# Kernel optimization log

Hardware: AMD Instinct MI355X
Metric: run time of the kernel (lower is better)

Reference implementation:

```python
import jax, jax.numpy as jnp
import numpy as np

D = 768    # text_feature_dim (BERT)
H = 1024   # hidden_dim
L = 16384  # history length


def setup_inputs() -> dict:
    key = jax.random.key(0)
    ks = jax.random.split(key, 10)
    text_v = jax.random.normal(ks[0], (1, D), dtype=jnp.float32)
    result = jax.random.uniform(ks[1], (1,), dtype=jnp.float32)
    text_s = jax.random.normal(ks[2], (L, D), dtype=jnp.float32)
    hidden_s = jax.random.normal(ks[3], (L, H), dtype=jnp.float32)
    # GRU params (PyTorch layout: W_ih [3H, 2D], W_hh [3H, H]), uniform(-1/sqrt(H), 1/sqrt(H))
    s = 1.0 / np.sqrt(H)
    W_ih = jax.random.uniform(ks[4], (3 * H, 2 * D), minval=-s, maxval=s, dtype=jnp.float32)
    W_hh = jax.random.uniform(ks[5], (3 * H, H), minval=-s, maxval=s, dtype=jnp.float32)
    b_ih = jax.random.uniform(ks[6], (3 * H,), minval=-s, maxval=s, dtype=jnp.float32)
    b_hh = jax.random.uniform(ks[7], (3 * H,), minval=-s, maxval=s, dtype=jnp.float32)
    # score layer: Linear(D+H, 1)
    s2 = 1.0 / np.sqrt(D + H)
    score_W = jax.random.uniform(ks[8], (1, D + H), minval=-s2, maxval=s2, dtype=jnp.float32)
    score_b = jax.random.uniform(ks[9], (1,), minval=-s2, maxval=s2, dtype=jnp.float32)
    return {"text_v": text_v, "result": result, "text_s": text_s, "hidden_s": hidden_s,
            "W_ih": W_ih, "W_hh": W_hh, "b_ih": b_ih, "b_hh": b_hh,
            "score_W": score_W, "score_b": score_b}


def reference(text_v, result, text_s, hidden_s, W_ih, W_hh, b_ih, b_hh, score_W, score_b):
    # --- attention over growing history ---
    h = hidden_s[-1:, :]                                   # [1, H] last hidden state
    alpha = jax.nn.softmax(text_s @ text_v.T, axis=0)      # [L, 1]
    attn_h = alpha.T @ hidden_s                            # [1, H]

    # --- score prediction ---
    pred_v = jnp.concatenate([text_v, attn_h], axis=1)     # [1, D+H]
    score = pred_v @ score_W.T + score_b                   # [1, 1]

    # --- input gating by correctness ---
    zeros = jnp.zeros_like(text_v)
    x_r = jnp.where(result >= 0.5,
                    jnp.concatenate([text_v, zeros], axis=1),
                    jnp.concatenate([zeros, text_v], axis=1))  # [1, 2D]

    # --- GRU cell (PyTorch gate order: r, z, n) ---
    gi = x_r @ W_ih.T + b_ih                               # [1, 3H]
    gh = h @ W_hh.T + b_hh                                 # [1, 3H]
    i_r, i_z, i_n = jnp.split(gi, 3, axis=1)
    h_r, h_z, h_n = jnp.split(gh, 3, axis=1)
    r = jax.nn.sigmoid(i_r + h_r)
    z = jax.nn.sigmoid(i_z + h_z)
    n = jnp.tanh(i_n + r * h_n)
    h_new = (1.0 - z) * n + z * h                          # [1, H]

    return score[0], h_new                                 # score.squeeze(0) -> [1]
```

## Files before the change

kernel.cpp:

```cpp
#include <hip/hip_runtime.h>
#include <math.h>

#define LL 16384
#define Dm 768
#define Hm 1024

#define WS_DOTS  0
#define WS_STATS 16384
#define WS_GI    16400
#define WS_GH    19472
#define WS_PART  24576
#define WS_PART2 (24576 + 512*1024)

__device__ __forceinline__ float dot4(float4 a, float4 b) {
    return a.x*b.x + a.y*b.y + a.z*b.z + a.w*b.w;
}

__global__ __launch_bounds__(256) void k_dots_gigh(
    const float* __restrict__ text_v, const float* __restrict__ result,
    const float* __restrict__ text_s, const float* __restrict__ hidden_s,
    const float* __restrict__ W_ih, const float* __restrict__ W_hh,
    const float* __restrict__ b_ih, const float* __restrict__ b_hh,
    float* __restrict__ ws)
{
    const int tid  = threadIdx.x;
    const int lane = tid & 63;
    const int wv   = tid >> 6;
    const int b    = blockIdx.x;

    if (b < 1024) {
        const int wave_g = b*4 + wv;
        float4 tv0 = *(const float4*)(text_v + 4*lane);
        float4 tv1 = *(const float4*)(text_v + 4*lane + 256);
        float4 tv2 = *(const float4*)(text_v + 4*lane + 512);
        #pragma unroll
        for (int r = 0; r < 4; ++r) {
            const int row = wave_g*4 + r;
            const float* p = text_s + (size_t)row*Dm + 4*lane;
            float4 x0 = *(const float4*)(p);
            float4 x1 = *(const float4*)(p + 256);
            float4 x2 = *(const float4*)(p + 512);
            float s = dot4(x0, tv0) + dot4(x1, tv1) + dot4(x2, tv2);
            #pragma unroll
            for (int o = 32; o; o >>= 1) s += __shfl_xor(s, o);
            if (lane == 0) ws[WS_DOTS + row] = s;
        }
    } else if (b < 1216) {
        const int wave_g = (b - 1024)*4 + wv;
        const int off = (result[0] >= 0.5f) ? 0 : Dm;
        float4 tv0 = *(const float4*)(text_v + 4*lane);
        float4 tv1 = *(const float4*)(text_v + 4*lane + 256);
        float4 tv2 = *(const float4*)(text_v + 4*lane + 512);
        #pragma unroll
        for (int r = 0; r < 4; ++r) {
            const int k = wave_g*4 + r;
            const float* p = W_ih + (size_t)k*(2*Dm) + off + 4*lane;
            float4 x0 = *(const float4*)(p);
            float4 x1 = *(const float4*)(p + 256);
            float4 x2 = *(const float4*)(p + 512);
            float s = dot4(x0, tv0) + dot4(x1, tv1) + dot4(x2, tv2);
            #pragma unroll
            for (int o = 32; o; o >>= 1) s += __shfl_xor(s, o);
            if (lane == 0) ws[WS_GI + k] = s + b_ih[k];
        }
    } else {
        const int wave_g = (b - 1216)*4 + wv;
        const float* h = hidden_s + (size_t)(LL - 1)*Hm;
        float4 h0 = *(const float4*)(h + 4*lane);
        float4 h1 = *(const float4*)(h + 4*lane + 256);
        float4 h2 = *(const float4*)(h + 4*lane + 512);
        float4 h3 = *(const float4*)(h + 4*lane + 768);
        #pragma unroll
        for (int r = 0; r < 4; ++r) {
            const int k = wave_g*4 + r;
            const float* p = W_hh + (size_t)k*Hm + 4*lane;
            float4 x0 = *(const float4*)(p);
            float4 x1 = *(const float4*)(p + 256);
            float4 x2 = *(const float4*)(p + 512);
            float4 x3 = *(const float4*)(p + 768);
            float s = dot4(x0, h0) + dot4(x1, h1) + dot4(x2, h2) + dot4(x3, h3);
            #pragma unroll
            for (int o = 32; o; o >>= 1) s += __shfl_xor(s, o);
            if (lane == 0) ws[WS_GH + k] = s + b_hh[k];
        }
    }
}

__global__ __launch_bounds__(1024) void k_stats(float* __restrict__ ws) {
    __shared__ float red[16];
    __shared__ float s_m;
    const int tid = threadIdx.x;
    const float* dots = ws + WS_DOTS;
    float v[16];
    float m = -1e30f;
    #pragma unroll
    for (int k = 0; k < 16; ++k) { v[k] = dots[tid + k*1024]; m = fmaxf(m, v[k]); }
    #pragma unroll
    for (int o = 32; o; o >>= 1) m = fmaxf(m, __shfl_xor(m, o));
    if ((tid & 63) == 0) red[tid >> 6] = m;
    __syncthreads();
    if (tid == 0) {
        float mm = red[0];
        #pragma unroll
        for (int i = 1; i < 16; ++i) mm = fmaxf(mm, red[i]);
        s_m = mm;
    }
    __syncthreads();
    m = s_m;
    float s = 0.f;
    #pragma unroll
    for (int k = 0; k < 16; ++k) s += expf(v[k] - m);
    #pragma unroll
    for (int o = 32; o; o >>= 1) s += __shfl_xor(s, o);
    if ((tid & 63) == 0) red[tid >> 6] = s;
    __syncthreads();
    if (tid == 0) {
        float ss = 0.f;
        #pragma unroll
        for (int i = 0; i < 16; ++i) ss += red[i];
        ws[WS_STATS]     = s_m;
        ws[WS_STATS + 1] = 1.0f / ss;
    }
}

__global__ __launch_bounds__(256) void k_wsum(
    const float* __restrict__ hidden_s, float* __restrict__ ws)
{
    const int p = blockIdx.x;
    const int t = threadIdx.x;
    const float m   = ws[WS_STATS];
    const float inv = ws[WS_STATS + 1];
    float4 acc = {0.f, 0.f, 0.f, 0.f};
    const int row0 = p*32;
    for (int r = 0; r < 32; ++r) {
        const int row = row0 + r;
        const float w = expf(ws[WS_DOTS + row] - m) * inv;
        const float4 hv = *(const float4*)(hidden_s + (size_t)row*Hm + 4*t);
        acc.x += w*hv.x; acc.y += w*hv.y; acc.z += w*hv.z; acc.w += w*hv.w;
    }
    *(float4*)(ws + WS_PART + p*1024 + 4*t) = acc;
}

__global__ __launch_bounds__(256) void k_reduce(float* __restrict__ ws) {
    const int b = blockIdx.x;
    const int t = threadIdx.x;
    float4 acc = {0.f, 0.f, 0.f, 0.f};
    for (int r = 0; r < 32; ++r) {
        const float4 v = *(const float4*)(ws + WS_PART + (size_t)(b*32 + r)*1024 + 4*t);
        acc.x += v.x; acc.y += v.y; acc.z += v.z; acc.w += v.w;
    }
    *(float4*)(ws + WS_PART2 + b*1024 + 4*t) = acc;
}

__global__ __launch_bounds__(1024) void k_final(
    const float* __restrict__ text_v, const float* __restrict__ hidden_s,
    const float* __restrict__ score_W, const float* __restrict__ score_b,
    float* __restrict__ ws, float* __restrict__ out)
{
    __shared__ float sred[16];
    const int tid = threadIdx.x;
    float a = 0.f;
    #pragma unroll
    for (int r = 0; r < 16; ++r) a += ws[WS_PART2 + r*1024 + tid];
    float sp = a * score_W[Dm + tid];
    if (tid < Dm) sp += text_v[tid] * score_W[tid];
    #pragma unroll
    for (int o = 32; o; o >>= 1) sp += __shfl_xor(sp, o);
    if ((tid & 63) == 0) sred[tid >> 6] = sp;
    __syncthreads();
    if (tid == 0) {
        float s = score_b[0];
        #pragma unroll
        for (int i = 0; i < 16; ++i) s += sred[i];
        out[0] = s;
    }
    const float gi_r = ws[WS_GI + tid];
    const float gi_z = ws[WS_GI + 1024 + tid];
    const float gi_n = ws[WS_GI + 2048 + tid];
    const float gh_r = ws[WS_GH + tid];
    const float gh_z = ws[WS_GH + 1024 + tid];
    const float gh_n = ws[WS_GH + 2048 + tid];
    const float hprev = hidden_s[(size_t)(LL - 1)*Hm + tid];
    const float r = 1.f / (1.f + expf(-(gi_r + gh_r)));
    const float z = 1.f / (1.f + expf(-(gi_z + gh_z)));
    const float n = tanhf(gi_n + r*gh_n);
    out[1 + tid] = (1.f - z)*n + z*hprev;
}

extern "C" void kernel_launch(void* const* d_in, const int* in_sizes, int n_in,
                              void* d_out, int out_size, void* d_ws, size_t ws_size,
                              hipStream_t stream) {
    const float* text_v   = (const float*)d_in[0];
    const float* result   = (const float*)d_in[1];
    const float* text_s   = (const float*)d_in[2];
    const float* hidden_s = (const float*)d_in[3];
    const float* W_ih     = (const float*)d_in[4];
    const float* W_hh     = (const float*)d_in[5];
    const float* b_ih     = (const float*)d_in[6];
    const float* b_hh     = (const float*)d_in[7];
    const float* score_W  = (const float*)d_in[8];
    const float* score_b  = (const float*)d_in[9];
    float* out = (float*)d_out;
    float* ws  = (float*)d_ws;

    k_dots_gigh<<<1408, 256, 0, stream>>>(text_v, result, text_s, hidden_s,
                                          W_ih, W_hh, b_ih, b_hh, ws);
    k_stats <<<1,   1024, 0, stream>>>(ws);
    k_wsum  <<<512, 256,  0, stream>>>(hidden_s, ws);
    k_reduce<<<16,  256,  0, stream>>>(ws);
    k_final <<<1,   1024, 0, stream>>>(text_v, hidden_s, score_W, score_b, ws, out);
}
```

Before: 192.2 us.

## Fuse attention dots and weighted sum with online-softmax partial reductions

Replaces the global two-pass softmax (dots kernel, stats kernel, weighted-sum kernel) with a flash-style online softmax. Each block computes dots for its 32 rows, a local max and exp-weights, and the weighted hidden-state sum in one pass, storing partial max, sum and vector. The partials are then merged hierarchically with rescaling in the mid and final kernels. This removes two launches and the global round trip of the dot products, and lets text_s and hidden_s reads share one kernel. The GI/GH block counts are also rebalanced to fewer blocks with more rows each.

```diff
diff --git a/kernel.cpp b/kernel.cpp
--- a/kernel.cpp
+++ b/kernel.cpp
@@ -5,55 +5,84 @@
 #define Dm 768
 #define Hm 1024
 
-#define WS_DOTS  0
-#define WS_STATS 16384
-#define WS_GI    16400
-#define WS_GH    19472
-#define WS_PART  24576
-#define WS_PART2 (24576 + 512*1024)
+#define ATT_B 512
+#define GI_B  48
+#define GH_B  64
+
+#define WS_GI 0
+#define WS_GH 3072
+#define WS_PM 6144
+#define WS_PS 6656
+#define WS_PV 7168
+#define WS_M2 (7168 + 512*1024)
+#define WS_S2 (WS_M2 + 16)
+#define WS_V2 (WS_S2 + 16)
 
 __device__ __forceinline__ float dot4(float4 a, float4 b) {
     return a.x*b.x + a.y*b.y + a.z*b.z + a.w*b.w;
 }
 
-__global__ __launch_bounds__(256) void k_dots_gigh(
+__global__ __launch_bounds__(256) void k_main(
     const float* __restrict__ text_v, const float* __restrict__ result,
     const float* __restrict__ text_s, const float* __restrict__ hidden_s,
     const float* __restrict__ W_ih, const float* __restrict__ W_hh,
     const float* __restrict__ b_ih, const float* __restrict__ b_hh,
     float* __restrict__ ws)
 {
+    const int b    = blockIdx.x;
     const int tid  = threadIdx.x;
     const int lane = tid & 63;
     const int wv   = tid >> 6;
-    const int b    = blockIdx.x;
-
-    if (b < 1024) {
-        const int wave_g = b*4 + wv;
+
+    if (b < ATT_B) {
+        __shared__ float dots[32];
+        __shared__ float wts[32];
+        const int row0 = b * 32;
         float4 tv0 = *(const float4*)(text_v + 4*lane);
         float4 tv1 = *(const float4*)(text_v + 4*lane + 256);
         float4 tv2 = *(const float4*)(text_v + 4*lane + 512);
         #pragma unroll
-        for (int r = 0; r < 4; ++r) {
-            const int row = wave_g*4 + r;
-            const float* p = text_s + (size_t)row*Dm + 4*lane;
+        for (int i = 0; i < 8; ++i) {
+            const int rl = wv*8 + i;
+            const float* p = text_s + (size_t)(row0 + rl)*Dm + 4*lane;
             float4 x0 = *(const float4*)(p);
             float4 x1 = *(const float4*)(p + 256);
             float4 x2 = *(const float4*)(p + 512);
             float s = dot4(x0, tv0) + dot4(x1, tv1) + dot4(x2, tv2);
             #pragma unroll
             for (int o = 32; o; o >>= 1) s += __shfl_xor(s, o);
-            if (lane == 0) ws[WS_DOTS + row] = s;
-        }
-    } else if (b < 1216) {
-        const int wave_g = (b - 1024)*4 + wv;
+            if (lane == 0) dots[rl] = s;
+        }
+        __syncthreads();
+        float m = dots[0];
+        #pragma unroll
+        for (int r = 1; r < 32; ++r) m = fmaxf(m, dots[r]);
+        if (tid < 32) wts[tid] = expf(dots[tid] - m);
+        __syncthreads();
+        float4 acc = {0.f, 0.f, 0.f, 0.f};
+        for (int r = 0; r < 32; ++r) {
+            const float w = wts[r];
+            const float4 hv = *(const float4*)(hidden_s + (size_t)(row0 + r)*Hm + 4*tid);
+            acc.x += w*hv.x; acc.y += w*hv.y; acc.z += w*hv.z; acc.w += w*hv.w;
+        }
+        *(float4*)(ws + WS_PV + (size_t)b*1024 + 4*tid) = acc;
+        if (tid == 0) {
+            float s = 0.f;
+            #pragma unroll
+            for (int r = 0; r < 32; ++r) s += wts[r];
+            ws[WS_PM + b] = m;
+            ws[WS_PS + b] = s;
+        }
+    } else if (b < ATT_B + GI_B) {
+        const int gb = b - ATT_B;
         const int off = (result[0] >= 0.5f) ? 0 : Dm;
         float4 tv0 = *(const float4*)(text_v + 4*lane);
         float4 tv1 = *(const float4*)(text_v + 4*lane + 256);
         float4 tv2 = *(const float4*)(text_v + 4*lane + 512);
-        #pragma unroll
-        for (int r = 0; r < 4; ++r) {
-            const int k = wave_g*4 + r;
+        const int kbase = gb*64 + wv*16;
+        #pragma unroll
+        for (int i = 0; i < 16; ++i) {
+            const int k = kbase + i;
             const float* p = W_ih + (size_t)k*(2*Dm) + off + 4*lane;
             float4 x0 = *(const float4*)(p);
             float4 x1 = *(const float4*)(p + 256);
@@ -64,15 +93,16 @@
             if (lane == 0) ws[WS_GI + k] = s + b_ih[k];
         }
     } else {
-        const int wave_g = (b - 1216)*4 + wv;
+        const int hb = b - ATT_B - GI_B;
         const float* h = hidden_s + (size_t)(LL - 1)*Hm;
         float4 h0 = *(const float4*)(h + 4*lane);
         float4 h1 = *(const float4*)(h + 4*lane + 256);
         float4 h2 = *(const float4*)(h + 4*lane + 512);
         float4 h3 = *(const float4*)(h + 4*lane + 768);
-        #pragma unroll
-        for (int r = 0; r < 4; ++r) {
-            const int k = wave_g*4 + r;
+        const int kbase = hb*48 + wv*12;
+        #pragma unroll
+        for (int i = 0; i < 12; ++i) {
+            const int k = kbase + i;
             const float* p = W_hh + (size_t)k*Hm + 4*lane;
             float4 x0 = *(const float4*)(p);
             float4 x1 = *(const float4*)(p + 256);
@@ -86,70 +116,30 @@
     }
 }
 
-__global__ __launch_bounds__(1024) void k_stats(float* __restrict__ ws) {
-    __shared__ float red[16];
-    __shared__ float s_m;
-    const int tid = threadIdx.x;
-    const float* dots = ws + WS_DOTS;
-    float v[16];
-    float m = -1e30f;
-    #pragma unroll
-    for (int k = 0; k < 16; ++k) { v[k] = dots[tid + k*1024]; m = fmaxf(m, v[k]); }
-    #pragma unroll
-    for (int o = 32; o; o >>= 1) m = fmaxf(m, __shfl_xor(m, o));
-    if ((tid & 63) == 0) red[tid >> 6] = m;
-    __syncthreads();
-    if (tid == 0) {
-        float mm = red[0];
-        #pragma unroll
-        for (int i = 1; i < 16; ++i) mm = fmaxf(mm, red[i]);
-        s_m = mm;
-    }
-    __syncthreads();
-    m = s_m;
-    float s = 0.f;
-    #pragma unroll
-    for (int k = 0; k < 16; ++k) s += expf(v[k] - m);
-    #pragma unroll
-    for (int o = 32; o; o >>= 1) s += __shfl_xor(s, o);
-    if ((tid & 63) == 0) red[tid >> 6] = s;
-    __syncthreads();
-    if (tid == 0) {
-        float ss = 0.f;
-        #pragma unroll
-        for (int i = 0; i < 16; ++i) ss += red[i];
-        ws[WS_STATS]     = s_m;
-        ws[WS_STATS + 1] = 1.0f / ss;
-    }
-}
-
-__global__ __launch_bounds__(256) void k_wsum(
-    const float* __restrict__ hidden_s, float* __restrict__ ws)
-{
-    const int p = blockIdx.x;
-    const int t = threadIdx.x;
-    const float m   = ws[WS_STATS];
-    const float inv = ws[WS_STATS + 1];
-    float4 acc = {0.f, 0.f, 0.f, 0.f};
-    const int row0 = p*32;
-    for (int r = 0; r < 32; ++r) {
-        const int row = row0 + r;
-        const float w = expf(ws[WS_DOTS + row] - m) * inv;
-        const float4 hv = *(const float4*)(hidden_s + (size_t)row*Hm + 4*t);
-        acc.x += w*hv.x; acc.y += w*hv.y; acc.z += w*hv.z; acc.w += w*hv.w;
-    }
-    *(float4*)(ws + WS_PART + p*1024 + 4*t) = acc;
-}
-
-__global__ __launch_bounds__(256) void k_reduce(float* __restrict__ ws) {
+__global__ __launch_bounds__(256) void k_mid(float* __restrict__ ws) {
+    __shared__ float sc[32];
     const int b = blockIdx.x;
     const int t = threadIdx.x;
+    const int p0 = b * 32;
+    float m = ws[WS_PM + p0];
+    #pragma unroll
+    for (int r = 1; r < 32; ++r) m = fmaxf(m, ws[WS_PM + p0 + r]);
+    if (t < 32) sc[t] = expf(ws[WS_PM + p0 + t] - m);
+    __syncthreads();
     float4 acc = {0.f, 0.f, 0.f, 0.f};
     for (int r = 0; r < 32; ++r) {
-        const float4 v = *(const float4*)(ws + WS_PART + (size_t)(b*32 + r)*1024 + 4*t);
-        acc.x += v.x; acc.y += v.y; acc.z += v.z; acc.w += v.w;
-    }
-    *(float4*)(ws + WS_PART2 + b*1024 + 4*t) = acc;
+        const float w = sc[r];
+        const float4 v = *(const float4*)(ws + WS_PV + (size_t)(p0 + r)*1024 + 4*t);
+        acc.x += w*v.x; acc.y += w*v.y; acc.z += w*v.z; acc.w += w*v.w;
+    }
+    *(float4*)(ws + WS_V2 + (size_t)b*1024 + 4*t) = acc;
+    if (t == 0) {
+        float s = 0.f;
+        #pragma unroll
+        for (int r = 0; r < 32; ++r) s += sc[r] * ws[WS_PS + p0 + r];
+        ws[WS_M2 + b] = m;
+        ws[WS_S2 + b] = s;
+    }
 }
 
 __global__ __launch_bounds__(1024) void k_final(
@@ -159,9 +149,17 @@
 {
     __shared__ float sred[16];
     const int tid = threadIdx.x;
-    float a = 0.f;
-    #pragma unroll
-    for (int r = 0; r < 16; ++r) a += ws[WS_PART2 + r*1024 + tid];
+    float M = ws[WS_M2];
+    #pragma unroll
+    for (int r = 1; r < 16; ++r) M = fmaxf(M, ws[WS_M2 + r]);
+    float S = 0.f, a = 0.f;
+    #pragma unroll
+    for (int r = 0; r < 16; ++r) {
+        const float scl = expf(ws[WS_M2 + r] - M);
+        S += scl * ws[WS_S2 + r];
+        a += scl * ws[WS_V2 + r*1024 + tid];
+    }
+    a /= S;
     float sp = a * score_W[Dm + tid];
     if (tid < Dm) sp += text_v[tid] * score_W[tid];
     #pragma unroll
@@ -203,10 +201,8 @@
     float* out = (float*)d_out;
     float* ws  = (float*)d_ws;
 
-    k_dots_gigh<<<1408, 256, 0, stream>>>(text_v, result, text_s, hidden_s,
-                                          W_ih, W_hh, b_ih, b_hh, ws);
-    k_stats <<<1,   1024, 0, stream>>>(ws);
-    k_wsum  <<<512, 256,  0, stream>>>(hidden_s, ws);
-    k_reduce<<<16,  256,  0, stream>>>(ws);
-    k_final <<<1,   1024, 0, stream>>>(text_v, hidden_s, score_W, score_b, ws, out);
-}
+    k_main <<<ATT_B + GI_B + GH_B, 256, 0, stream>>>(
+        text_v, result, text_s, hidden_s, W_ih, W_hh, b_ih, b_hh, ws);
+    k_mid  <<<16, 256,  0, stream>>>(ws);
+    k_final<<<1,  1024, 0, stream>>>(text_v, hidden_s, score_W, score_b, ws, out);
+}
```

Result: no change. 194.5 us (+1.2%).
